# Optimization experiments

Measured on AMD Instinct MI355X. Metric: run time of the kernel, lower is better.

The kernel has to match this reference:

```python
import jax, jax.numpy as jnp
import numpy as np

LN_EPS = 1e-5

def _layernorm(x, g, b):
    mu = jnp.mean(x, axis=-1, keepdims=True)
    var = jnp.var(x, axis=-1, keepdims=True)
    return (x - mu) * jax.lax.rsqrt(var + LN_EPS) * g + b

def setup_inputs() -> dict:
    key = jax.random.key(0)
    ks = jax.random.split(key, 8)
    B, N, n, m, a = 4096, 50000, 1024, 16384, 256
    return {
        "x": jax.random.normal(ks[0], (B, n), dtype=jnp.float32),
        "X_data": jax.random.normal(ks[1], (N, n), dtype=jnp.float32),
        "memory_indices": jax.random.randint(ks[2], (m,), 0, N, dtype=jnp.int64)
            if jax.config.jax_enable_x64 else jax.random.randint(ks[2], (m,), 0, N, dtype=jnp.int32),
        "W_q": jax.random.normal(ks[3], (a, n), dtype=jnp.float32) / np.sqrt(n),
        "W_k": jax.random.normal(ks[4], (a, n), dtype=jnp.float32) / np.sqrt(n),
        "W_v": jax.random.normal(ks[5], (n, n), dtype=jnp.float32) / np.sqrt(n),
        "g_q": jnp.ones((a,), jnp.float32), "b_q": jnp.zeros((a,), jnp.float32),
        "g_k": jnp.ones((a,), jnp.float32), "b_k": jnp.zeros((a,), jnp.float32),
        "g_v": jnp.ones((n,), jnp.float32), "b_v": jnp.zeros((n,), jnp.float32),
    }

def reference(x, X_data, memory_indices, W_q, W_k, W_v, g_q, b_q, g_k, b_k, g_v, b_v):
    # Gather memory bank rows: [m, n]
    X_cross = X_data[memory_indices]
    n = x.shape[-1]
    # preprocess(): scalar normalizer so mean row norm ~= sqrt(n) (SAE convention)
    C = jnp.mean(jnp.linalg.norm(X_cross, axis=-1)) / jnp.sqrt(jnp.asarray(n, x.dtype))
    X_cross = X_cross / C
    xs = x / C
    # QKV projections (Linear, no bias) + per-stream LayerNorm
    q = _layernorm(xs @ W_q.T, g_q, b_q)        # [B, a]
    k = _layernorm(X_cross @ W_k.T, g_k, b_k)   # [m, a]
    v = _layernorm(X_cross @ W_v.T, g_v, b_v)   # [m, n]
    # scaled dot-product attention over the memory bank
    scale = 1.0 / np.sqrt(q.shape[-1])
    attn = jax.nn.softmax(jnp.einsum('ba,ma->bm', q, k) * scale, axis=-1)  # [B, m]
    x_hat = attn @ v                             # [B, n]
    return (xs, x_hat, attn, v)
```

## Files before the change

kernel.cpp:

```cpp
#include <hip/hip_runtime.h>
#include <math.h>

typedef _Float16 hlf4 __attribute__((ext_vector_type(4)));
typedef _Float16 hlf8 __attribute__((ext_vector_type(8)));
typedef float f32x4 __attribute__((ext_vector_type(4)));

static __device__ __forceinline__ float blk_sum(float v) {
    __shared__ float sm[256];
    int tid = threadIdx.x;
    sm[tid] = v; __syncthreads();
#pragma unroll
    for (int s = 128; s > 0; s >>= 1) {
        if (tid < s) sm[tid] += sm[tid + s];
        __syncthreads();
    }
    float r = sm[0]; __syncthreads();
    return r;
}

static __device__ __forceinline__ float blk_max(float v) {
    __shared__ float sm[256];
    int tid = threadIdx.x;
    sm[tid] = v; __syncthreads();
#pragma unroll
    for (int s = 128; s > 0; s >>= 1) {
        if (tid < s) sm[tid] = fmaxf(sm[tid], sm[tid + s]);
        __syncthreads();
    }
    float r = sm[0]; __syncthreads();
    return r;
}

__global__ __launch_bounds__(256) void k_row_norms(
    const float* __restrict__ X, const int* __restrict__ idx,
    float* __restrict__ norms, int n) {
    long long r = idx[blockIdx.x];
    const float* xr = X + r * (long long)n;
    float s = 0.f;
    for (int k = threadIdx.x * 4; k < n; k += 256 * 4) {
        float4 v = *(const float4*)(xr + k);
        s = fmaf(v.x, v.x, s); s = fmaf(v.y, v.y, s);
        s = fmaf(v.z, v.z, s); s = fmaf(v.w, v.w, s);
    }
    float tot = blk_sum(s);
    if (threadIdx.x == 0) norms[blockIdx.x] = sqrtf(tot);
}

__global__ __launch_bounds__(256) void k_cinv(
    const float* __restrict__ norms, int m, int n, float* __restrict__ cinv) {
    float s = 0.f;
    for (int i = threadIdx.x; i < m; i += 256) s += norms[i];
    float tot = blk_sum(s);
    if (threadIdx.x == 0) cinv[0] = (float)m * sqrtf((float)n) / tot;
}

__global__ __launch_bounds__(256) void k_scale2(
    const float* __restrict__ x, const float* __restrict__ cinv,
    float* __restrict__ y, _Float16* __restrict__ yh, long long total4) {
    float c = cinv[0];
    long long i = blockIdx.x * 256ll + threadIdx.x;
    long long stride = (long long)gridDim.x * 256ll;
    for (; i < total4; i += stride) {
        float4 v = ((const float4*)x)[i];
        v.x *= c; v.y *= c; v.z *= c; v.w *= c;
        ((float4*)y)[i] = v;
        hlf4 o = {(_Float16)v.x, (_Float16)v.y, (_Float16)v.z, (_Float16)v.w};
        ((hlf4*)yh)[i] = o;
    }
}

__global__ __launch_bounds__(256) void k_gather_cvt(
    const float* __restrict__ X, const int* __restrict__ idx,
    const float* __restrict__ cinv, _Float16* __restrict__ out, int n) {
    long long r = idx[blockIdx.x];
    float c = cinv[0];
    const float* src = X + r * (long long)n;
    _Float16* dst = out + (long long)blockIdx.x * n;
    for (int k = threadIdx.x * 4; k < n; k += 256 * 4) {
        float4 v = *(const float4*)(src + k);
        hlf4 o = {(_Float16)(v.x * c), (_Float16)(v.y * c),
                  (_Float16)(v.z * c), (_Float16)(v.w * c)};
        *(hlf4*)(dst + k) = o;
    }
}

__global__ __launch_bounds__(256) void k_cvt(
    const float* __restrict__ in, _Float16* __restrict__ out, long long n4) {
    long long i = blockIdx.x * 256ll + threadIdx.x;
    long long stride = (long long)gridDim.x * 256ll;
    for (; i < n4; i += stride) {
        float4 v = ((const float4*)in)[i];
        hlf4 o = {(_Float16)v.x, (_Float16)v.y, (_Float16)v.z, (_Float16)v.w};
        ((hlf4*)out)[i] = o;
    }
}

__global__ __launch_bounds__(256) void k_tcvt(
    const float* __restrict__ in, _Float16* __restrict__ out, int R, int Cc) {
    __shared__ _Float16 t[32][34];
    int tx = threadIdx.x & 31, ty = threadIdx.x >> 5;
    int c0 = blockIdx.x * 32, r0 = blockIdx.y * 32;
#pragma unroll
    for (int i = 0; i < 32; i += 8)
        t[ty + i][tx] = (_Float16)in[(long long)(r0 + ty + i) * Cc + c0 + tx];
    __syncthreads();
#pragma unroll
    for (int i = 0; i < 32; i += 8)
        out[(long long)(c0 + ty + i) * R + r0 + tx] = t[tx][ty + i];
}

template <typename T>
static __device__ __forceinline__ hlf8 ld8(const T* p) {
    if constexpr (sizeof(T) == 4) {
        float4 a = *(const float4*)(p + 0);
        float4 b = *(const float4*)(p + 4);
        hlf8 r = {(_Float16)a.x, (_Float16)a.y, (_Float16)a.z, (_Float16)a.w,
                  (_Float16)b.x, (_Float16)b.y, (_Float16)b.z, (_Float16)b.w};
        return r;
    } else {
        return *(const hlf8*)p;
    }
}

#define GLDH 40
template <typename TA, typename TB>
__global__ __launch_bounds__(512) void k_gemm8(
    const TA* __restrict__ A, int lda,
    const TB* __restrict__ B, int ldb,
    float* __restrict__ Cc, long long ldc, int K,
    float* __restrict__ part, long long zstride) {
    __shared__ _Float16 Ah[2][128 * GLDH];
    __shared__ _Float16 Bh[2][128 * GLDH];
    const int tid = threadIdx.x;
    const long long m0 = (long long)blockIdx.x * 128;
    const long long n0 = (long long)blockIdx.y * 128;
    const int KC = K / gridDim.z;
    const int kbase = blockIdx.z * KC;
    const int srow = tid >> 2, sseg = tid & 3;
    const TA* Ap = A + (m0 + srow) * lda + kbase + sseg * 8;
    const TB* Bp = B + (n0 + srow) * ldb + kbase + sseg * 8;
    const int lane = tid & 63, wv = tid >> 6;
    const int wm = (wv >> 2) * 64, wn = (wv & 3) * 32;
    const int fr = lane & 15, fq = lane >> 4;
    const int sOff = srow * GLDH + sseg * 8;

    f32x4 acc[4][2] = {};
    hlf8 ra, rb;

    ra = ld8(Ap); rb = ld8(Bp);
    *(hlf8*)&Ah[0][sOff] = ra; *(hlf8*)&Bh[0][sOff] = rb;
    __syncthreads();

    const int NT = KC / 32;
    for (int kt = 0; kt < NT; ++kt) {
        const int cur = kt & 1;
        if (kt + 1 < NT) {
            ra = ld8(Ap + (long long)(kt + 1) * 32);
            rb = ld8(Bp + (long long)(kt + 1) * 32);
        }
        hlf8 af[4], bf[2];
#pragma unroll
        for (int i = 0; i < 4; ++i)
            af[i] = *(const hlf8*)&Ah[cur][(wm + i * 16 + fr) * GLDH + fq * 8];
#pragma unroll
        for (int j = 0; j < 2; ++j)
            bf[j] = *(const hlf8*)&Bh[cur][(wn + j * 16 + fr) * GLDH + fq * 8];
#pragma unroll
        for (int i = 0; i < 4; ++i)
#pragma unroll
            for (int j = 0; j < 2; ++j)
                acc[i][j] = __builtin_amdgcn_mfma_f32_16x16x32_f16(af[i], bf[j], acc[i][j], 0, 0, 0);
        if (kt + 1 < NT) {
            const int nx = cur ^ 1;
            *(hlf8*)&Ah[nx][sOff] = ra; *(hlf8*)&Bh[nx][sOff] = rb;
        }
        __syncthreads();
    }

    float* out = (gridDim.z == 1) ? Cc : (part + (long long)blockIdx.z * zstride);
#pragma unroll
    for (int i = 0; i < 4; ++i)
#pragma unroll
        for (int j = 0; j < 2; ++j) {
            float* cp = out + (m0 + wm + i * 16 + fq * 4) * ldc + (n0 + wn + j * 16 + fr);
#pragma unroll
            for (int r = 0; r < 4; ++r) cp[(long long)r * ldc] = acc[i][j][r];
        }
}

__global__ __launch_bounds__(256) void k_redux(
    const float* __restrict__ part, float* __restrict__ out,
    long long n4, long long zs4, int Z) {
    long long i = blockIdx.x * 256ll + threadIdx.x;
    long long stride = (long long)gridDim.x * 256ll;
    for (; i < n4; i += stride) {
        float4 s = ((const float4*)part)[i];
        for (int z = 1; z < Z; ++z) {
            float4 t = ((const float4*)part)[i + z * zs4];
            s.x += t.x; s.y += t.y; s.z += t.z; s.w += t.w;
        }
        ((float4*)out)[i] = s;
    }
}

template <int CNT>
__global__ __launch_bounds__(256) void k_layernorm(
    float* __restrict__ Y, const float* __restrict__ g,
    const float* __restrict__ b, int W) {
    float* yr = Y + (long long)blockIdx.x * W;
    float v[CNT];
    float s = 0.f;
#pragma unroll
    for (int i = 0; i < CNT; ++i) {
        v[i] = yr[threadIdx.x + (i << 8)];
        s += v[i];
    }
    float mu = blk_sum(s) / (float)W;
    float sq = 0.f;
#pragma unroll
    for (int i = 0; i < CNT; ++i) {
        float d = v[i] - mu;
        sq = fmaf(d, d, sq);
    }
    float var = blk_sum(sq) / (float)W;
    float rs = rsqrtf(var + 1e-5f);
#pragma unroll
    for (int i = 0; i < CNT; ++i) {
        int col = threadIdx.x + (i << 8);
        yr[col] = (v[i] - mu) * rs * g[col] + b[col];
    }
}

__global__ __launch_bounds__(256) void k_softmax(
    float* __restrict__ S, _Float16* __restrict__ Sh, float scale) {
    float* sr = S + (long long)blockIdx.x * 16384;
    _Float16* shr = Sh ? Sh + (long long)blockIdx.x * 16384 : nullptr;
    float4 r[16];
    float mx = -1e30f;
#pragma unroll
    for (int i = 0; i < 16; ++i) {
        float4 t = ((const float4*)sr)[threadIdx.x + (i << 8)];
        t.x *= scale; t.y *= scale; t.z *= scale; t.w *= scale;
        r[i] = t;
        mx = fmaxf(mx, fmaxf(fmaxf(t.x, t.y), fmaxf(t.z, t.w)));
    }
    mx = blk_max(mx);
    float sum = 0.f;
#pragma unroll
    for (int i = 0; i < 16; ++i) {
        float4 t = r[i];
        t.x = __expf(t.x - mx); t.y = __expf(t.y - mx);
        t.z = __expf(t.z - mx); t.w = __expf(t.w - mx);
        r[i] = t;
        sum += t.x + t.y + t.z + t.w;
    }
    sum = blk_sum(sum);
    float inv = 1.0f / sum;
#pragma unroll
    for (int i = 0; i < 16; ++i) {
        float4 t = r[i];
        t.x *= inv; t.y *= inv; t.z *= inv; t.w *= inv;
        ((float4*)sr)[threadIdx.x + (i << 8)] = t;
        if (shr) {
            hlf4 o = {(_Float16)t.x, (_Float16)t.y, (_Float16)t.z, (_Float16)t.w};
            ((hlf4*)shr)[threadIdx.x + (i << 8)] = o;
        }
    }
}

extern "C" void kernel_launch(void* const* d_in, const int* in_sizes, int n_in,
                              void* d_out, int out_size, void* d_ws, size_t ws_size,
                              hipStream_t stream) {
    const float* x      = (const float*)d_in[0];
    const float* X_data = (const float*)d_in[1];
    const int*   midx   = (const int*)d_in[2];
    const float* W_q    = (const float*)d_in[3];
    const float* W_k    = (const float*)d_in[4];
    const float* W_v    = (const float*)d_in[5];
    const float* g_q    = (const float*)d_in[6];
    const float* b_q    = (const float*)d_in[7];
    const float* g_k    = (const float*)d_in[8];
    const float* b_k    = (const float*)d_in[9];
    const float* g_v    = (const float*)d_in[10];
    const float* b_v    = (const float*)d_in[11];

    const int n  = in_sizes[10];
    const int a  = in_sizes[6];
    const int m  = in_sizes[2];
    const int Bn = in_sizes[0] / n;

    float* out  = (float*)d_out;
    float* xs   = out;
    float* xhat = xs + (long long)Bn * n;
    float* attn = xhat + (long long)Bn * n;
    float* vout = attn + (long long)Bn * m;

    char* wp = (char*)d_ws;
    auto carve = [&](size_t bytes) -> char* {
        char* r = wp; wp += (bytes + 255) & ~(size_t)255; return r;
    };
    float*     norms = (float*)carve((size_t)m * 4);
    float*     cinv  = (float*)carve(16);
    char*      alias0 = wp;
    float*     qmat  = (float*)carve((size_t)Bn * a * 4);
    float*     kmat  = (float*)carve((size_t)m * a * 4);
    _Float16*  xs_h  = (_Float16*)carve((size_t)Bn * n * 2);
    _Float16*  Xc_h  = (_Float16*)carve((size_t)m * n * 2);
    _Float16*  Wq_h  = (_Float16*)carve((size_t)a * n * 2);
    _Float16*  Wk_h  = (_Float16*)carve((size_t)a * n * 2);
    _Float16*  Wv_h  = (_Float16*)carve((size_t)n * n * 2);
    _Float16*  q_h   = (_Float16*)carve((size_t)Bn * a * 2);
    _Float16*  k_h   = (_Float16*)carve((size_t)m * a * 2);
    float*     splitk = (float*)alias0;
    const int  SK = 4;
    _Float16*  vT_h  = (_Float16*)carve((size_t)n * m * 2);
    size_t used = (size_t)(wp - (char*)d_ws);
    _Float16* attn_h = nullptr;
    if (ws_size >= used + (size_t)Bn * m * 2 + 256)
        attn_h = (_Float16*)carve((size_t)Bn * m * 2);

    hipLaunchKernelGGL(k_row_norms, dim3(m), dim3(256), 0, stream, X_data, midx, norms, n);
    hipLaunchKernelGGL(k_cinv, dim3(1), dim3(256), 0, stream, norms, m, n, cinv);

    hipLaunchKernelGGL(k_scale2, dim3(2048), dim3(256), 0, stream,
                       x, cinv, xs, xs_h, (long long)Bn * n / 4);
    hipLaunchKernelGGL(k_gather_cvt, dim3(m), dim3(256), 0, stream,
                       X_data, midx, cinv, Xc_h, n);

    hipLaunchKernelGGL(k_cvt, dim3(256), dim3(256), 0, stream, W_q, Wq_h, (long long)a * n / 4);
    hipLaunchKernelGGL(k_cvt, dim3(256), dim3(256), 0, stream, W_k, Wk_h, (long long)a * n / 4);
    hipLaunchKernelGGL(k_cvt, dim3(1024), dim3(256), 0, stream, W_v, Wv_h, (long long)n * n / 4);

    hipLaunchKernelGGL((k_gemm8<_Float16, _Float16>), dim3(Bn / 128, a / 128), dim3(512), 0, stream,
                       xs_h, n, Wq_h, n, qmat, a, n, (float*)nullptr, 0ll);
    hipLaunchKernelGGL((k_gemm8<_Float16, _Float16>), dim3(m / 128, a / 128), dim3(512), 0, stream,
                       Xc_h, n, Wk_h, n, kmat, a, n, (float*)nullptr, 0ll);
    hipLaunchKernelGGL((k_gemm8<_Float16, _Float16>), dim3(m / 128, n / 128), dim3(512), 0, stream,
                       Xc_h, n, Wv_h, n, vout, n, n, (float*)nullptr, 0ll);

    hipLaunchKernelGGL(k_layernorm<1>, dim3(Bn), dim3(256), 0, stream, qmat, g_q, b_q, a);
    hipLaunchKernelGGL(k_layernorm<1>, dim3(m),  dim3(256), 0, stream, kmat, g_k, b_k, a);
    hipLaunchKernelGGL(k_layernorm<4>, dim3(m),  dim3(256), 0, stream, vout, g_v, b_v, n);
    hipLaunchKernelGGL(k_cvt, dim3(1024), dim3(256), 0, stream, qmat, q_h, (long long)Bn * a / 4);
    hipLaunchKernelGGL(k_cvt, dim3(4096), dim3(256), 0, stream, kmat, k_h, (long long)m * a / 4);
    hipLaunchKernelGGL(k_tcvt, dim3(n / 32, m / 32), dim3(256), 0, stream, vout, vT_h, m, n);

    hipLaunchKernelGGL((k_gemm8<_Float16, _Float16>), dim3(Bn / 128, m / 128), dim3(512), 0, stream,
                       q_h, a, k_h, a, attn, m, a, (float*)nullptr, 0ll);
    float sc = 1.0f / sqrtf((float)a);
    hipLaunchKernelGGL(k_softmax, dim3(Bn), dim3(256), 0, stream, attn, attn_h, sc);

    long long zstride = (long long)Bn * n;
    if (attn_h)
        hipLaunchKernelGGL((k_gemm8<_Float16, _Float16>), dim3(Bn / 128, n / 128, SK), dim3(512), 0, stream,
                           attn_h, m, vT_h, m, xhat, n, m, splitk, zstride);
    else
        hipLaunchKernelGGL((k_gemm8<float, _Float16>), dim3(Bn / 128, n / 128, SK), dim3(512), 0, stream,
                           attn, m, vT_h, m, xhat, n, m, splitk, zstride);
    hipLaunchKernelGGL(k_redux, dim3(2048), dim3(256), 0, stream,
                       splitk, xhat, (long long)Bn * n / 4, zstride / 4, SK);
}
```

Before: 669.3 us.

## Add direct global-to-LDS GEMM kernel with XOR swizzle and larger warp tiles

Adds a new 256-thread fp16 GEMM kernel that uses global_load_lds to copy tiles straight into shared memory, bypassing registers. The LDS layout uses an XOR swizzle instead of padding to avoid bank conflicts. Each wave now computes a 64x64 tile rather than 64x32, raising MFMA work per LDS read. All fp16 GEMMs switch to this kernel, and the old kernel is kept only for the fp32-attn fallback. This costs more accumulator registers and relies on the intrinsic's per-wave contiguous LDS write pattern being mapped correctly.

```diff
diff --git a/kernel.cpp b/kernel.cpp
--- a/kernel.cpp
+++ b/kernel.cpp
@@ -4,6 +4,12 @@
 typedef _Float16 hlf4 __attribute__((ext_vector_type(4)));
 typedef _Float16 hlf8 __attribute__((ext_vector_type(8)));
 typedef float f32x4 __attribute__((ext_vector_type(4)));
+
+static __device__ __forceinline__ void gl_lds16(const void* g, void* l) {
+    __builtin_amdgcn_global_load_lds(
+        (const __attribute__((address_space(1))) unsigned int*)g,
+        (__attribute__((address_space(3))) unsigned int*)l, 16, 0, 0);
+}
 
 static __device__ __forceinline__ float blk_sum(float v) {
     __shared__ float sm[256];
@@ -109,9 +115,86 @@
         out[(long long)(c0 + ty + i) * R + r0 + tx] = t[tx][ty + i];
 }
 
-template <typename T>
-static __device__ __forceinline__ hlf8 ld8(const T* p) {
-    if constexpr (sizeof(T) == 4) {
+__global__ __launch_bounds__(256) void k_gemm4(
+    const _Float16* __restrict__ A, int lda,
+    const _Float16* __restrict__ B, int ldb,
+    float* __restrict__ Cc, long long ldc, int K,
+    float* __restrict__ part, long long zstride) {
+    __shared__ _Float16 Ah[2][4096];
+    __shared__ _Float16 Bh[2][4096];
+    const int tid = threadIdx.x;
+    const long long m0 = (long long)blockIdx.x * 128;
+    const long long n0 = (long long)blockIdx.y * 128;
+    const int KC = K / gridDim.z;
+    const int kbase = blockIdx.z * KC;
+    const int lane = tid & 63, wv = tid >> 6;
+    const int wm = (wv >> 1) * 64, wn = (wv & 1) * 64;
+    const int fr = lane & 15, fq = lane >> 4;
+
+    const int s0 = tid, s1 = tid + 256;
+    const int r0s = s0 >> 2, r1s = s1 >> 2;
+    const int g0 = (((s0 & 3) ^ (r0s & 3)) << 3);
+    const int g1 = (((s1 & 3) ^ (r1s & 3)) << 3);
+    const _Float16* A0 = A + (m0 + r0s) * (long long)lda + kbase + g0;
+    const _Float16* A1 = A + (m0 + r1s) * (long long)lda + kbase + g1;
+    const _Float16* B0 = B + (n0 + r0s) * (long long)ldb + kbase + g0;
+    const _Float16* B1 = B + (n0 + r1s) * (long long)ldb + kbase + g1;
+
+    f32x4 acc[4][4] = {};
+
+    const int NT = KC / 32;
+    {
+        gl_lds16(A0, &Ah[0][wv * 512]);
+        gl_lds16(A1, &Ah[0][2048 + wv * 512]);
+        gl_lds16(B0, &Bh[0][wv * 512]);
+        gl_lds16(B1, &Bh[0][2048 + wv * 512]);
+    }
+    __syncthreads();
+
+    for (int kt = 0; kt < NT; ++kt) {
+        const int cur = kt & 1;
+        if (kt + 1 < NT) {
+            const int nx = cur ^ 1;
+            const long long ko = (long long)(kt + 1) * 32;
+            gl_lds16(A0 + ko, &Ah[nx][wv * 512]);
+            gl_lds16(A1 + ko, &Ah[nx][2048 + wv * 512]);
+            gl_lds16(B0 + ko, &Bh[nx][wv * 512]);
+            gl_lds16(B1 + ko, &Bh[nx][2048 + wv * 512]);
+        }
+        hlf8 af[4], bf[4];
+#pragma unroll
+        for (int i = 0; i < 4; ++i) {
+            const int r = wm + i * 16 + fr;
+            af[i] = *(const hlf8*)&Ah[cur][r * 32 + ((fq ^ (r & 3)) << 3)];
+        }
+#pragma unroll
+        for (int j = 0; j < 4; ++j) {
+            const int r = wn + j * 16 + fr;
+            bf[j] = *(const hlf8*)&Bh[cur][r * 32 + ((fq ^ (r & 3)) << 3)];
+        }
+#pragma unroll
+        for (int i = 0; i < 4; ++i)
+#pragma unroll
+            for (int j = 0; j < 4; ++j)
+                acc[i][j] = __builtin_amdgcn_mfma_f32_16x16x32_f16(af[i], bf[j], acc[i][j], 0, 0, 0);
+        __syncthreads();
+    }
+
+    float* outp = (gridDim.z == 1) ? Cc : (part + (long long)blockIdx.z * zstride);
+#pragma unroll
+    for (int i = 0; i < 4; ++i)
+#pragma unroll
+        for (int j = 0; j < 4; ++j) {
+            float* cp = outp + (m0 + wm + i * 16 + fq * 4) * ldc + (n0 + wn + j * 16 + fr);
+#pragma unroll
+            for (int r = 0; r < 4; ++r) cp[(long long)r * ldc] = acc[i][j][r];
+        }
+}
+
+#define GLDH 40
+template <typename TA>
+static __device__ __forceinline__ hlf8 ld8f(const TA* p) {
+    if constexpr (sizeof(TA) == 4) {
         float4 a = *(const float4*)(p + 0);
         float4 b = *(const float4*)(p + 4);
         hlf8 r = {(_Float16)a.x, (_Float16)a.y, (_Float16)a.z, (_Float16)a.w,
@@ -122,11 +205,10 @@
     }
 }
 
-#define GLDH 40
-template <typename TA, typename TB>
+template <typename TA>
 __global__ __launch_bounds__(512) void k_gemm8(
     const TA* __restrict__ A, int lda,
-    const TB* __restrict__ B, int ldb,
+    const _Float16* __restrict__ B, int ldb,
     float* __restrict__ Cc, long long ldc, int K,
     float* __restrict__ part, long long zstride) {
     __shared__ _Float16 Ah[2][128 * GLDH];
@@ -137,8 +219,8 @@
     const int KC = K / gridDim.z;
     const int kbase = blockIdx.z * KC;
     const int srow = tid >> 2, sseg = tid & 3;
-    const TA* Ap = A + (m0 + srow) * lda + kbase + sseg * 8;
-    const TB* Bp = B + (n0 + srow) * ldb + kbase + sseg * 8;
+    const TA* Ap = A + (m0 + srow) * (long long)lda + kbase + sseg * 8;
+    const _Float16* Bp = B + (n0 + srow) * (long long)ldb + kbase + sseg * 8;
     const int lane = tid & 63, wv = tid >> 6;
     const int wm = (wv >> 2) * 64, wn = (wv & 3) * 32;
     const int fr = lane & 15, fq = lane >> 4;
@@ -146,8 +228,7 @@
 
     f32x4 acc[4][2] = {};
     hlf8 ra, rb;
-
-    ra = ld8(Ap); rb = ld8(Bp);
+    ra = ld8f(Ap); rb = ld8f(Bp);
     *(hlf8*)&Ah[0][sOff] = ra; *(hlf8*)&Bh[0][sOff] = rb;
     __syncthreads();
 
@@ -155,8 +236,8 @@
     for (int kt = 0; kt < NT; ++kt) {
         const int cur = kt & 1;
         if (kt + 1 < NT) {
-            ra = ld8(Ap + (long long)(kt + 1) * 32);
-            rb = ld8(Bp + (long long)(kt + 1) * 32);
+            ra = ld8f(Ap + (long long)(kt + 1) * 32);
+            rb = ld8f(Bp + (long long)(kt + 1) * 32);
         }
         hlf8 af[4], bf[2];
 #pragma unroll
@@ -177,12 +258,12 @@
         __syncthreads();
     }
 
-    float* out = (gridDim.z == 1) ? Cc : (part + (long long)blockIdx.z * zstride);
+    float* outp = (gridDim.z == 1) ? Cc : (part + (long long)blockIdx.z * zstride);
 #pragma unroll
     for (int i = 0; i < 4; ++i)
 #pragma unroll
         for (int j = 0; j < 2; ++j) {
-            float* cp = out + (m0 + wm + i * 16 + fq * 4) * ldc + (n0 + wn + j * 16 + fr);
+            float* cp = outp + (m0 + wm + i * 16 + fq * 4) * ldc + (n0 + wn + j * 16 + fr);
 #pragma unroll
             for (int r = 0; r < 4; ++r) cp[(long long)r * ldc] = acc[i][j][r];
         }
@@ -331,11 +412,11 @@
     hipLaunchKernelGGL(k_cvt, dim3(256), dim3(256), 0, stream, W_k, Wk_h, (long long)a * n / 4);
     hipLaunchKernelGGL(k_cvt, dim3(1024), dim3(256), 0, stream, W_v, Wv_h, (long long)n * n / 4);
 
-    hipLaunchKernelGGL((k_gemm8<_Float16, _Float16>), dim3(Bn / 128, a / 128), dim3(512), 0, stream,
+    hipLaunchKernelGGL(k_gemm4, dim3(Bn / 128, a / 128), dim3(256), 0, stream,
                        xs_h, n, Wq_h, n, qmat, a, n, (float*)nullptr, 0ll);
-    hipLaunchKernelGGL((k_gemm8<_Float16, _Float16>), dim3(m / 128, a / 128), dim3(512), 0, stream,
+    hipLaunchKernelGGL(k_gemm4, dim3(m / 128, a / 128), dim3(256), 0, stream,
                        Xc_h, n, Wk_h, n, kmat, a, n, (float*)nullptr, 0ll);
-    hipLaunchKernelGGL((k_gemm8<_Float16, _Float16>), dim3(m / 128, n / 128), dim3(512), 0, stream,
+    hipLaunchKernelGGL(k_gemm4, dim3(m / 128, n / 128), dim3(256), 0, stream,
                        Xc_h, n, Wv_h, n, vout, n, n, (float*)nullptr, 0ll);
 
     hipLaunchKernelGGL(k_layernorm<1>, dim3(Bn), dim3(256), 0, stream, qmat, g_q, b_q, a);
@@ -345,18 +426,19 @@
     hipLaunchKernelGGL(k_cvt, dim3(4096), dim3(256), 0, stream, kmat, k_h, (long long)m * a / 4);
     hipLaunchKernelGGL(k_tcvt, dim3(n / 32, m / 32), dim3(256), 0, stream, vout, vT_h, m, n);
 
-    hipLaunchKernelGGL((k_gemm8<_Float16, _Float16>), dim3(Bn / 128, m / 128), dim3(512), 0, stream,
+    hipLaunchKernelGGL(k_gemm4, dim3(Bn / 128, m / 128), dim3(256), 0, stream,
                        q_h, a, k_h, a, attn, m, a, (float*)nullptr, 0ll);
     float sc = 1.0f / sqrtf((float)a);
     hipLaunchKernelGGL(k_softmax, dim3(Bn), dim3(256), 0, stream, attn, attn_h, sc);
 
     long long zstride = (long long)Bn * n;
-    if (attn_h)
-        hipLaunchKernelGGL((k_gemm8<_Float16, _Float16>), dim3(Bn / 128, n / 128, SK), dim3(512), 0, stream,
+    if (attn_h) {
+        hipLaunchKernelGGL(k_gemm4, dim3(Bn / 128, n / 128, SK), dim3(256), 0, stream,
                            attn_h, m, vT_h, m, xhat, n, m, splitk, zstride);
-    else
-        hipLaunchKernelGGL((k_gemm8<float, _Float16>), dim3(Bn / 128, n / 128, SK), dim3(512), 0, stream,
+    } else {
+        hipLaunchKernelGGL((k_gemm8<float>), dim3(Bn / 128, n / 128, SK), dim3(512), 0, stream,
                            attn, m, vT_h, m, xhat, n, m, splitk, zstride);
+    }
     hipLaunchKernelGGL(k_redux, dim3(2048), dim3(256), 0, stream,
                        splitk, xhat, (long long)Bn * n / 4, zstride / 4, SK);
 }
```

Measured after the change: 629.3 us. -6.0%, faster.
